# Kernel tuning notes

Measured on AMD Instinct MI355X. Metric: run time of the kernel, lower is better.

The kernel has to match this reference:

```python
import jax, jax.numpy as jnp
import numpy as np

B, S, HD, NH, AH, F = 64, 256, 512, 8, 256, 2
DH = HD // NH          # item/pos head dim = 64
DA = AH // NH          # attribute head dim = 32
EPS = 1e-12


def setup_inputs() -> dict:
    key = jax.random.key(0)
    ks = iter(jax.random.split(key, 32))
    rn = lambda shape, s=1.0: jax.random.normal(next(ks), shape, dtype=jnp.float32) * s
    w = 0.02
    return {
        "input_tensor": rn((B, S, HD)),
        "attribute_table": rn((B, S, 1, AH)),
        "position_embedding": rn((B, S, HD)),
        "Wq": rn((HD, HD), w), "bq": jnp.zeros((HD,), jnp.float32),
        "Wk": rn((HD, HD), w), "bk": jnp.zeros((HD,), jnp.float32),
        "Wv": rn((HD, HD), w), "bv": jnp.zeros((HD,), jnp.float32),
        "Wqp": rn((HD, HD), w), "bqp": jnp.zeros((HD,), jnp.float32),
        "Wkp": rn((HD, HD), w), "bkp": jnp.zeros((HD,), jnp.float32),
        "Wqa": rn((F, AH, AH), w), "bqa": jnp.zeros((F, AH), jnp.float32),
        "Wka": rn((F, AH, AH), w), "bka": jnp.zeros((F, AH), jnp.float32),
        "fw1": rn((S, S), w), "fb1": jnp.zeros((S,), jnp.float32),
        "fw2": rn((1, S), w), "fb2": jnp.zeros((1,), jnp.float32),
        "Wd": rn((HD, HD), w), "bd": jnp.zeros((HD,), jnp.float32),
        "gamma": jnp.ones((HD,), jnp.float32),
        "beta": jnp.zeros((HD,), jnp.float32),
    }


def _split_heads(x, nh):
    b, s, h = x.shape
    return x.reshape(b, s, nh, h // nh).transpose(0, 2, 1, 3)  # [B,H,S,d]


def reference(input_tensor, attribute_table, position_embedding,
              Wq, bq, Wk, bk, Wv, bv, Wqp, bqp, Wkp, bkp,
              Wqa, bqa, Wka, bka, fw1, fb1, fw2, fb2,
              Wd, bd, gamma, beta):
    q = _split_heads(input_tensor @ Wq.T + bq, NH)
    k = _split_heads(input_tensor @ Wk.T + bk, NH)
    v = _split_heads(input_tensor @ Wv.T + bv, NH)
    qp = _split_heads(position_embedding @ Wqp.T + bqp, NH)
    kp = _split_heads(position_embedding @ Wkp.T + bkp, NH)

    item_scores = jnp.einsum('bhqd,bhkd->bhqk', q, k)
    pos_scores = jnp.einsum('bhqd,bhkd->bhqk', qp, kp)

    attr = attribute_table.squeeze(-2)                       # [B,S,AH]
    qa = jnp.einsum('bsc,foc->fbso', attr, Wqa) + bqa[:, None, None, :]
    ka = jnp.einsum('bsc,foc->fbso', attr, Wka) + bka[:, None, None, :]
    qa = qa.reshape(F, B, S, NH, DA).transpose(0, 1, 3, 2, 4)  # [F,B,H,S,da]
    ka = ka.reshape(F, B, S, NH, DA).transpose(0, 1, 3, 2, 4)
    attr_scores = jnp.einsum('fbhqd,fbhkd->fbhqk', qa, ka)
    attr_scores = attr_scores.transpose(1, 2, 3, 0, 4)         # [B,H,S,F,S]

    # gate fusion (VanillaAttention over the F+2 score sources)
    stacked = jnp.concatenate(
        [attr_scores, item_scores[..., None, :], pos_scores[..., None, :]],
        axis=-2)                                               # [B,H,S,F+2,S]
    energy = jnp.maximum(stacked @ fw1.T + fb1, 0.0) @ fw2.T + fb2
    gate_w = jax.nn.softmax(energy.squeeze(-1), axis=-1)        # [B,H,S,F+2]
    scores = jnp.sum(stacked * gate_w[..., None], axis=-2)      # [B,H,S,S]

    scores = scores / np.sqrt(DH).astype(np.float32)
    probs = jax.nn.softmax(scores, axis=-1)
    ctx = jnp.einsum('bhqk,bhkd->bhqd', probs, v)
    ctx = ctx.transpose(0, 2, 1, 3).reshape(B, S, HD)

    h = ctx @ Wd.T + bd
    x = h + input_tensor
    mu = jnp.mean(x, axis=-1, keepdims=True)
    var = jnp.mean(jnp.square(x - mu), axis=-1, keepdims=True)
    return gamma * (x - mu) / jnp.sqrt(var + EPS) + beta
```

## Files before the change

### kernel.cpp

```cpp
#include <hip/hip_runtime.h>

typedef unsigned short u16;
typedef unsigned int   u32;
typedef __bf16 bf16x8 __attribute__((ext_vector_type(8)));
typedef float  f32x4  __attribute__((ext_vector_type(4)));
typedef u16    u16x4  __attribute__((ext_vector_type(4)));
typedef u16    u16x8  __attribute__((ext_vector_type(8)));

#define BB 64
#define SS 256
#define HDIM 512
#define NHEAD 8
#define BS (BB*SS)
#define NBH 512

__device__ __forceinline__ u16 f2bf(float f){
    u32 u = __builtin_bit_cast(u32, f);
    u32 r = u + 0x7FFFu + ((u>>16)&1u);
    return (u16)(r>>16);
}
__device__ __forceinline__ float bf2f(u16 u){
    return __builtin_bit_cast(float, (u32)u<<16);
}
__device__ __forceinline__ void gload16(const void* g, void* l){
    __builtin_amdgcn_global_load_lds(
        (const __attribute__((address_space(1))) void*)g,
        (__attribute__((address_space(3))) void*)l, 16, 0, 0);
}

__device__ __forceinline__ size_t zrow(int bh, int s){
    return ((size_t)bh*256 + s)*384;
}

__global__ __launch_bounds__(256) void cvt_k(const float* __restrict__ s,
                                             u16* __restrict__ d, int n8)
{
    int i = blockIdx.x*256 + threadIdx.x;
    const int stride = gridDim.x*256;
    for (; i < n8; i += stride) {
        f32x4 a = ((const f32x4*)s)[i*2];
        f32x4 b = ((const f32x4*)s)[i*2+1];
        u16x8 o = { f2bf(a[0]),f2bf(a[1]),f2bf(a[2]),f2bf(a[3]),
                    f2bf(b[0]),f2bf(b[1]),f2bf(b[2]),f2bf(b[3]) };
        ((u16x8*)d)[i] = o;
    }
}

__global__ __launch_bounds__(256) void cvtW_k(
    const float* __restrict__ Wq,  const float* __restrict__ Wk,
    const float* __restrict__ Wv,  const float* __restrict__ Wqp,
    const float* __restrict__ Wkp, const float* __restrict__ Wqa,
    const float* __restrict__ Wka, const float* __restrict__ Wd,
    u16* __restrict__ dst)
{
    const int i = blockIdx.x*256 + threadIdx.x;
    const float* s; u16* d; int local;
    if (i < 163840) {
        const int seg = i >> 15; local = i & 32767;
        s = seg==0?Wq:seg==1?Wk:seg==2?Wv:seg==3?Wqp:Wkp;
        d = dst + (size_t)seg*262144;
    } else if (i < 196608) {
        const int j = i - 163840; const int seg = j >> 14; local = j & 16383;
        s = seg ? Wka : Wqa;
        d = dst + 1310720 + (size_t)seg*131072;
    } else {
        local = i - 196608;
        s = Wd; d = dst + 1572864;
    }
    f32x4 a = ((const f32x4*)s)[local*2];
    f32x4 b = ((const f32x4*)s)[local*2+1];
    u16x8 o = { f2bf(a[0]),f2bf(a[1]),f2bf(a[2]),f2bf(a[3]),
                f2bf(b[0]),f2bf(b[1]),f2bf(b[2]),f2bf(b[3]) };
    ((u16x8*)d)[local] = o;
}

__global__ __launch_bounds__(64) void prep_fw1(const float* __restrict__ fw1,
                                               u16* __restrict__ fw1b)
{
    const int row = blockIdx.x;
    const int c0  = threadIdx.x * 4;
    float4 v = *(const float4*)(fw1 + (size_t)row*256 + c0);
    u16x4 pk = { f2bf(v.x), f2bf(v.y), f2bf(v.z), f2bf(v.w) };
    *(u16x4*)((char*)fw1b + (size_t)row*512 + ((c0*2) ^ ((row&7)<<4))) = pk;
}

template<int OUTMODE, int BBF16>
__global__ __launch_bounds__(256,3) void gemm128(
    const u16* __restrict__ A, const void* __restrict__ Bv,
    void* __restrict__ o0, void* __restrict__ o1, void* __restrict__ o2,
    const float* __restrict__ b0, const float* __restrict__ b1,
    const float* __restrict__ b2, const float* __restrict__ resid,
    int N, int K)
{
    __shared__ char sA[16384];
    __shared__ char sB[16384];
    const int tid = threadIdx.x, lane = tid & 63, w = tid >> 6;
    const int wr = (w & 1) * 64, wc = (w >> 1) * 64;
    const int flat = blockIdx.x;
    const int xcd = flat & 7, bi2 = flat >> 3;
    const int n_i = bi2 >> 4, mIn = bi2 & 15;
    const int m0 = (xcd*16 + mIn)*128, n0 = n_i*128;

    f32x4 acc[4][4];
    #pragma unroll
    for (int mi = 0; mi < 4; mi++)
        #pragma unroll
        for (int ni = 0; ni < 4; ni++) acc[mi][ni] = (f32x4){0.f,0.f,0.f,0.f};

    for (int k0 = 0; k0 < K; k0 += 64) {
        __syncthreads();
        #pragma unroll
        for (int i = 0; i < 4; i++) {
            const int off = w*4096 + i*1024 + lane*16;
            const int r = off >> 7, c = off & 0x70;
            gload16(A + (size_t)(m0 + r)*K + k0 + ((c ^ ((r&7)<<4)) >> 1),
                    sA + w*4096 + i*1024);
        }
        if (BBF16) {
            const u16* B = (const u16*)Bv;
            #pragma unroll
            for (int i = 0; i < 4; i++) {
                const int off = w*4096 + i*1024 + lane*16;
                const int r = off >> 7, c = off & 0x70;
                gload16(B + (size_t)(n0 + r)*K + k0 + ((c ^ ((r&7)<<4)) >> 1),
                        sB + w*4096 + i*1024);
            }
        } else {
            const float* B = (const float*)Bv;
            const int r = tid >> 1, cseg = (tid & 1) * 32;
            const float* p = B + (size_t)(n0 + r)*K + k0 + cseg;
            alignas(16) u16 tmp[32];
            #pragma unroll
            for (int j = 0; j < 8; j++) {
                float4 fv = ((const float4*)p)[j];
                tmp[j*4+0]=f2bf(fv.x); tmp[j*4+1]=f2bf(fv.y);
                tmp[j*4+2]=f2bf(fv.z); tmp[j*4+3]=f2bf(fv.w);
            }
            const int rx = (r&7)<<4;
            #pragma unroll
            for (int j = 0; j < 4; j++)
                *(u16x8*)(sB + r*128 + ((cseg*2 + j*16) ^ rx)) = *(u16x8*)(tmp + j*8);
        }
        __syncthreads();
        #pragma unroll
        for (int ks = 0; ks < 2; ks++) {
            const int kb = ks*64 + (lane>>4)*16;
            bf16x8 af[4], bf[4];
            #pragma unroll
            for (int mi = 0; mi < 4; mi++) {
                const int r = wr + mi*16 + (lane&15);
                af[mi] = *(const bf16x8*)(sA + r*128 + (kb ^ ((r&7)<<4)));
            }
            #pragma unroll
            for (int ni = 0; ni < 4; ni++) {
                const int r = wc + ni*16 + (lane&15);
                bf[ni] = *(const bf16x8*)(sB + r*128 + (kb ^ ((r&7)<<4)));
            }
            #pragma unroll
            for (int mi = 0; mi < 4; mi++)
                #pragma unroll
                for (int ni = 0; ni < 4; ni++)
                    acc[mi][ni] = __builtin_amdgcn_mfma_f32_16x16x32_bf16(
                        af[mi], bf[ni], acc[mi][ni], 0,0,0);
        }
    }
    #pragma unroll
    for (int mi = 0; mi < 4; mi++) {
        const int rowb = m0 + wr + mi*16 + (lane>>4)*4;
        const int bi = rowb >> 8, s0 = rowb & 255;
        #pragma unroll
        for (int ni = 0; ni < 4; ni++) {
            const int gn = n0 + wc + ni*16 + (lane&15);
            if (OUTMODE == 2) {
                float* out = (float*)o0;
                const float bb = b0[gn];
                #pragma unroll
                for (int r = 0; r < 4; r++) {
                    size_t idx = (size_t)(rowb+r)*N + gn;
                    out[idx] = acc[mi][ni][r] + bb + resid[idx];
                }
            } else if (OUTMODE == 4) {
                const int seg = gn >> 9, o = gn & 511;
                const int hh = o >> 6, d = o & 63;
                const float bb = (seg==0?b0:seg==1?b1:b2)[o];
                const int bh = bi*8 + hh;
                if (seg < 2) {
                    char* outp = (char*)(seg ? o1 : o0);
                    #pragma unroll
                    for (int r = 0; r < 4; r++) {
                        const int s = s0 + r;
                        *(u16*)(outp + zrow(bh,s) + ((d*2) ^ ((s&7)<<4)))
                            = f2bf(acc[mi][ni][r] + bb);
                    }
                } else {
                    u16x4 pk;
                    #pragma unroll
                    for (int r = 0; r < 4; r++) pk[r] = f2bf(acc[mi][ni][r] + bb);
                    *(u16x4*)((char*)o2 + (size_t)bh*32768 + d*512
                                        + ((s0*2) ^ ((d&7)<<4))) = pk;
                }
            } else if (OUTMODE == 5) {
                const int seg = gn >> 9, o = gn & 511;
                const int hh = o >> 6, d = o & 63;
                const float bb = (seg ? b1 : b0)[o];
                const int bh = bi*8 + hh;
                char* outp = (char*)(seg ? o1 : o0);
                #pragma unroll
                for (int r = 0; r < 4; r++) {
                    const int s = s0 + r;
                    *(u16*)(outp + zrow(bh,s) + (((64+d)*2) ^ ((s&7)<<4)))
                        = f2bf(acc[mi][ni][r] + bb);
                }
            } else {
                const int qk = gn >> 9, fo = gn & 511;
                const int f = fo >> 8, o = fo & 255;
                const int hh = o >> 5, d = o & 31;
                const int cb = 128 + f*32;
                const float bb = (qk ? b1 : b0)[fo];
                const int bh = bi*8 + hh;
                char* outp = (char*)(qk ? o1 : o0);
                #pragma unroll
                for (int r = 0; r < 4; r++) {
                    const int s = s0 + r;
                    *(u16*)(outp + zrow(bh,s) + (((cb+d)*2) ^ ((s&7)<<4)))
                        = f2bf(acc[mi][ni][r] + bb);
                }
            }
        }
    }
}

#define K34B_QZ   53248
#define K34B_QZSZ 13312
#define K34B_SMEM (53248 + 2*13312)

__global__ __launch_bounds__(512,4) void k34b(
    const u16* __restrict__ QZ, const u16* __restrict__ KZ,
    const u16* __restrict__ fw1b, const float* __restrict__ fb1,
    const float* __restrict__ fw2, float* __restrict__ e)
{
    extern __shared__ char sm[];
    const int tid = threadIdx.x, lane = tid & 63, w = tid >> 6;
    const int bh = blockIdx.x >> 1, sp = blockIdx.x & 1;
    const int l15 = lane & 15, lq = lane >> 4;
    const int base0 = sp ? 64 : 0;
    const int base1 = sp ? 160 : 128;

    auto stage_qz = [&](int qt4, int buf) {
        char* dst = sm + K34B_QZ + buf*K34B_QZSZ;
        {
            const int li = w*64 + lane;
            const int q = li / 13, c = li - q*13;
            const int cc = (c == 12) ? 0 : c;
            const int ld = cc*8;
            const int gd = (ld < 64) ? base0 + ld : base1 + (ld - 64);
            gload16((const char*)QZ + zrow(bh, qt4*64 + q)
                        + ((gd*2) ^ ((q&7)<<4)),
                    dst + w*1024);
        }
        if (w < 5) {
            const int li = 512 + w*64 + lane;
            const int q = li / 13, c = li - q*13;
            const int cc = (c == 12) ? 0 : c;
            const int ld = cc*8;
            const int gd = (ld < 64) ? base0 + ld : base1 + (ld - 64);
            gload16((const char*)QZ + zrow(bh, qt4*64 + q)
                        + ((gd*2) ^ ((q&7)<<4)),
                    dst + 8192 + w*1024);
        }
    };

    stage_qz(0, 0);
    {
        const int spair = tid & 127, dg = tid >> 7;
        const int s0 = spair*2;
        const char* r0 = (const char*)KZ + zrow(bh, s0);
        const char* r1 = (const char*)KZ + zrow(bh, s0+1);
        const int sw0 = (s0&7)<<4, sw1 = ((s0+1)&7)<<4;
        #pragma unroll
        for (int m = 0; m < 3; m++) {
            const int ld0 = dg*24 + m*8;
            const int gd = (ld0 < 64) ? base0 + ld0 : base1 + (ld0 - 64);
            u16x8 v0 = *(const u16x8*)(r0 + ((gd*2) ^ sw0));
            u16x8 v1 = *(const u16x8*)(r1 + ((gd*2) ^ sw1));
            #pragma unroll
            for (int ee = 0; ee < 8; ee++) {
                const int d = ld0 + ee;
                *(u32*)(sm + d*512 + ((s0*2) ^ ((d&7)<<4)))
                    = (u32)v0[ee] | ((u32)v1[ee] << 16);
            }
        }
    }
    __syncthreads();

    const int jb = w & 3, dh = w >> 2;
    f32x4 kacc[4][3];
    #pragma unroll
    for (int js = 0; js < 4; js++)
        #pragma unroll
        for (int ni = 0; ni < 3; ni++) kacc[js][ni] = (f32x4){0.f,0.f,0.f,0.f};
    #pragma unroll
    for (int ks = 0; ks < 8; ks++) {
        const int kb = ks*64 + lq*16;
        bf16x8 a[4];
        #pragma unroll
        for (int js = 0; js < 4; js++) {
            const int ar = jb*64 + js*16 + l15;
            a[js] = *(const bf16x8*)((const char*)fw1b + (size_t)ar*512
                                     + (kb ^ ((l15&7)<<4)));
        }
        #pragma unroll
        for (int ni = 0; ni < 3; ni++) {
            const int dr = dh*48 + ni*16 + l15;
            bf16x8 b = *(const bf16x8*)(sm + dr*512 + (kb ^ ((dr&7)<<4)));
            #pragma unroll
            for (int js = 0; js < 4; js++)
                kacc[js][ni] = __builtin_amdgcn_mfma_f32_16x16x32_bf16(
                    a[js], b, kacc[js][ni], 0,0,0);
        }
    }
    __syncthreads();

    #pragma unroll
    for (int js = 0; js < 4; js++)
        #pragma unroll
        for (int ni = 0; ni < 3; ni++) {
            const int d = dh*48 + ni*16 + l15;
            #pragma unroll
            for (int r = 0; r < 4; r++) {
                const int j = jb*64 + js*16 + lq*4 + r;
                *(u16*)(sm + j*208 + d*2) = f2bf(kacc[js][ni][r]);
            }
        }
    __syncthreads();

    const int qh = w >> 2;
    bf16x8 af2[4][3];
    #pragma unroll
    for (int js = 0; js < 4; js++) {
        const int ar = jb*64 + js*16 + l15;
        #pragma unroll
        for (int ks = 0; ks < 3; ks++)
            af2[js][ks] = *(const bf16x8*)(sm + ar*208 + ks*64 + lq*16);
    }
    float f1v[4][4], f2v[4][4];
    #pragma unroll
    for (int js = 0; js < 4; js++)
        #pragma unroll
        for (int r = 0; r < 4; r++) {
            const int j = jb*64 + js*16 + lq*4 + r;
            f1v[js][r] = fb1[j]; f2v[js][r] = fw2[j];
        }

    for (int qt = 0; qt < 4; qt++) {
        __syncthreads();
        if (qt < 3) stage_qz(qt+1, (qt+1)&1);
        const char* qb = sm + K34B_QZ + (qt&1)*K34B_QZSZ;
        #pragma unroll
        for (int qs = 0; qs < 2; qs++) {
            const int qoff = (qh*32 + qs*16 + l15)*208 + lq*16;
            f32x4 acc[4];
            #pragma unroll
            for (int js = 0; js < 4; js++) acc[js] = (f32x4){0.f,0.f,0.f,0.f};
            #pragma unroll
            for (int kk = 0; kk < 2; kk++) {
                bf16x8 b = *(const bf16x8*)(qb + qoff + kk*64);
                #pragma unroll
                for (int js = 0; js < 4; js++)
                    acc[js] = __builtin_amdgcn_mfma_f32_16x16x32_bf16(
                        af2[js][kk], b, acc[js], 0,0,0);
            }
            {
                float ep = 0.f;
                #pragma unroll
                for (int js = 0; js < 4; js++)
                    #pragma unroll
                    for (int r = 0; r < 4; r++)
                        ep += fmaxf(acc[js][r] + f1v[js][r], 0.f) * f2v[js][r];
                ep += __shfl_xor(ep, 16);
                ep += __shfl_xor(ep, 32);
                if (lane < 16)
                    ((float*)sm)[(jb*2 + 0)*256 + qt*64 + qh*32 + qs*16 + lane] = ep;
            }
            #pragma unroll
            for (int js = 0; js < 4; js++) acc[js] = (f32x4){0.f,0.f,0.f,0.f};
            {
                bf16x8 b = *(const bf16x8*)(qb + qoff + 128);
                #pragma unroll
                for (int js = 0; js < 4; js++)
                    acc[js] = __builtin_amdgcn_mfma_f32_16x16x32_bf16(
                        af2[js][2], b, acc[js], 0,0,0);
            }
            {
                float ep = 0.f;
                #pragma unroll
                for (int js = 0; js < 4; js++)
                    #pragma unroll
                    for (int r = 0; r < 4; r++)
                        ep += fmaxf(acc[js][r] + f1v[js][r], 0.f) * f2v[js][r];
                ep += __shfl_xor(ep, 16);
                ep += __shfl_xor(ep, 32);
                if (lane < 16)
                    ((float*)sm)[(jb*2 + 1)*256 + qt*64 + qh*32 + qs*16 + lane] = ep;
            }
        }
    }
    __syncthreads();
    {
        const int q = tid & 255, sl = tid >> 8;
        const float* el = (const float*)sm;
        float s = 0.f;
        #pragma unroll
        for (int j2 = 0; j2 < 4; j2++) s += el[(j2*2 + sl)*256 + q];
        const int gsrc = sl ? (2 + sp) : sp;
        e[((size_t)bh*256 + q)*4 + gsrc] = s;
    }
}

#define K5_KZ 24576
#define K5_VT 49152
#define K5_SMEM 81920

__global__ __launch_bounds__(256,2) void k5_mix(
    const u16* __restrict__ QZ, const u16* __restrict__ KZ,
    const u16* __restrict__ VT, const float* __restrict__ e,
    u16* __restrict__ ctx)
{
    extern __shared__ char sm[];
    const int tid = threadIdx.x, lane = tid & 63, w = tid >> 6;
    const int flat = blockIdx.x;
    const int xcd = flat & 7, idx = flat >> 3;
    const int qt = idx & 3;
    const int bh = (idx >> 2) * 8 + xcd;
    const int q0 = qt*64;
    const int b = bh >> 3, h = bh & 7;
    const int kq16 = (lane>>4)*16;

    #pragma unroll
    for (int i = 0; i < 6; i++)
        gload16((const char*)QZ + zrow(bh, q0) + i*4096 + w*1024 + lane*16,
                sm + i*4096 + w*1024);
    #pragma unroll
    for (int i = 0; i < 8; i++)
        gload16((const char*)VT + (size_t)bh*32768 + i*4096 + w*1024 + lane*16,
                sm + K5_VT + i*4096 + w*1024);
    #pragma unroll
    for (int i = 0; i < 6; i++)
        gload16((const char*)KZ + zrow(bh, 0) + i*4096 + w*1024 + lane*16,
                sm + K5_KZ + i*4096 + w*1024);
    __syncthreads();

    const int qrow = w*16 + (lane&15);
    float ga[4];
    {
        f32x4 ev = *(const f32x4*)(e + ((size_t)bh*256 + q0 + qrow)*4);
        float em = fmaxf(fmaxf(ev[0],ev[1]), fmaxf(ev[2],ev[3]));
        float s = 0.f;
        #pragma unroll
        for (int j = 0; j < 4; j++) { ga[j] = __expf(ev[j]-em); s += ga[j]; }
        const float gi = 1.f / s;
        #pragma unroll
        for (int j = 0; j < 4; j++) ga[j] *= gi;
    }
    const int asw = ((lane&15)&7) << 4;
    bf16x8 aF[6];
    #pragma unroll
    for (int ks = 0; ks < 6; ks++) {
        const int sidx = (ks<2)?0:(ks<4)?1:(ks<5)?2:3;
        u16x8 v = *(const u16x8*)(sm + qrow*384 + ((ks*64 + kq16) ^ asw));
        const float gg = ga[sidx];
        u16x8 pk;
        #pragma unroll
        for (int j = 0; j < 8; j++) pk[j] = f2bf(bf2f(v[j]) * gg);
        aF[ks] = __builtin_bit_cast(bf16x8, pk);
    }

    f32x4 macc[4][4];
    #pragma unroll
    for (int kt = 0; kt < 4; kt++)
        #pragma unroll
        for (int n = 0; n < 4; n++) macc[kt][n] = (f32x4){0.f,0.f,0.f,0.f};
    u16x8 kreg[6];
    #pragma unroll
    for (int kt = 0; kt < 4; kt++) {
        if (kt < 3) {
            #pragma unroll
            for (int j = 0; j < 6; j++)
                kreg[j] = *(const u16x8*)((const char*)KZ + zrow(bh, (kt+1)*64)
                                          + (tid + j*256)*16);
        }
        #pragma unroll
        for (int n = 0; n < 4; n++) {
            const int kr = n*16 + (lane&15);
            const int ksw = (kr&7)<<4;
            #pragma unroll
            for (int ks = 0; ks < 6; ks++) {
                bf16x8 bb = *(const bf16x8*)(sm + K5_KZ + kr*384 + ((ks*64 + kq16) ^ ksw));
                macc[kt][n] = __builtin_amdgcn_mfma_f32_16x16x32_bf16(
                    aF[ks], bb, macc[kt][n], 0,0,0);
            }
        }
        if (kt < 3) {
            __syncthreads();
            #pragma unroll
            for (int j = 0; j < 6; j++)
                *(u16x8*)(sm + K5_KZ + (tid + j*256)*16) = kreg[j];
            __syncthreads();
        }
    }
    __syncthreads();

    #pragma unroll
    for (int rr = 0; rr < 4; rr++) {
        float mx = -3.4e38f;
        #pragma unroll
        for (int kt = 0; kt < 4; kt++)
            #pragma unroll
            for (int n = 0; n < 4; n++) mx = fmaxf(mx, macc[kt][n][rr]);
        #pragma unroll
        for (int msk = 1; msk < 16; msk <<= 1) mx = fmaxf(mx, __shfl_xor(mx, msk));
        float s = 0.f;
        #pragma unroll
        for (int kt = 0; kt < 4; kt++)
            #pragma unroll
            for (int n = 0; n < 4; n++) {
                float pv = __expf((macc[kt][n][rr] - mx) * 0.125f);
                macc[kt][n][rr] = pv; s += pv;
            }
        #pragma unroll
        for (int msk = 1; msk < 16; msk <<= 1) s += __shfl_xor(s, msk);
        const float inv = 1.f / s;
        const int orow = w*16 + (lane>>4)*4 + rr;
        const int osw = (orow&7)<<4;
        #pragma unroll
        for (int kt = 0; kt < 4; kt++)
            #pragma unroll
            for (int n = 0; n < 4; n++) {
                const int col = kt*64 + n*16 + (lane&15);
                *(u16*)(sm + orow*512 + ((col*2) ^ osw)) = f2bf(macc[kt][n][rr]*inv);
            }
    }
    __syncthreads();

    f32x4 pacc[4];
    #pragma unroll
    for (int n = 0; n < 4; n++) pacc[n] = (f32x4){0.f,0.f,0.f,0.f};
    const int prow = w*16 + (lane&15);
    const int psw = ((lane&15)&7)<<4;
    #pragma unroll
    for (int ks = 0; ks < 8; ks++) {
        const int kb = ks*64 + kq16;
        bf16x8 a = *(const bf16x8*)(sm + prow*512 + (kb ^ psw));
        #pragma unroll
        for (int n = 0; n < 4; n++) {
            const int dr = n*16 + (lane&15);
            bf16x8 bb = *(const bf16x8*)(sm + K5_VT + dr*512 + (kb ^ ((dr&7)<<4)));
            pacc[n] = __builtin_amdgcn_mfma_f32_16x16x32_bf16(a, bb, pacc[n], 0,0,0);
        }
    }
    {
        const int orow = w*16 + (lane>>4)*4;
        #pragma unroll
        for (int n = 0; n < 4; n++) {
            const int d = n*16 + (lane&15);
            #pragma unroll
            for (int r = 0; r < 4; r++) {
                const size_t grow = (size_t)b*256 + q0 + orow + r;
                ctx[grow*512 + h*64 + d] = f2bf(pacc[n][r]);
            }
        }
    }
}

__global__ __launch_bounds__(256) void ln_k(float* __restrict__ x,
    const float* __restrict__ gamma, const float* __restrict__ beta)
{
    const int row = blockIdx.x*4 + (threadIdx.x >> 6);
    const int l = threadIdx.x & 63;
    float* p = x + (size_t)row*HDIM;
    f32x4 v0 = *(const f32x4*)(p + l*4);
    f32x4 v1 = *(const f32x4*)(p + 256 + l*4);
    float s = v0[0]+v0[1]+v0[2]+v0[3] + v1[0]+v1[1]+v1[2]+v1[3];
    #pragma unroll
    for (int msk = 1; msk < 64; msk <<= 1) s += __shfl_xor(s, msk);
    const float mu = s * (1.f/512.f);
    float vs = 0.f;
    #pragma unroll
    for (int j = 0; j < 4; j++) {
        float d0 = v0[j]-mu, d1 = v1[j]-mu;
        vs += d0*d0 + d1*d1;
    }
    #pragma unroll
    for (int msk = 1; msk < 64; msk <<= 1) vs += __shfl_xor(vs, msk);
    const float inv = 1.f / sqrtf(vs * (1.f/512.f) + 1e-12f);
    f32x4 o0, o1;
    #pragma unroll
    for (int j = 0; j < 4; j++) {
        o0[j] = gamma[l*4+j]     * (v0[j]-mu) * inv + beta[l*4+j];
        o1[j] = gamma[256+l*4+j] * (v1[j]-mu) * inv + beta[256+l*4+j];
    }
    *(f32x4*)(p + l*4) = o0;
    *(f32x4*)(p + 256 + l*4) = o1;
}

extern "C" void kernel_launch(void* const* d_in, const int* in_sizes, int n_in,
                              void* d_out, int out_size, void* d_ws, size_t ws_size,
                              hipStream_t stream)
{
    const float* input = (const float*)d_in[0];
    const float* attrt = (const float*)d_in[1];
    const float* pose  = (const float*)d_in[2];
    const float* Wq  = (const float*)d_in[3];  const float* bq  = (const float*)d_in[4];
    const float* Wk  = (const float*)d_in[5];  const float* bk  = (const float*)d_in[6];
    const float* Wv  = (const float*)d_in[7];  const float* bv  = (const float*)d_in[8];
    const float* Wqp = (const float*)d_in[9];  const float* bqp = (const float*)d_in[10];
    const float* Wkp = (const float*)d_in[11]; const float* bkp = (const float*)d_in[12];
    const float* Wqa = (const float*)d_in[13]; const float* bqa = (const float*)d_in[14];
    const float* Wka = (const float*)d_in[15]; const float* bka = (const float*)d_in[16];
    const float* fw1 = (const float*)d_in[17]; const float* fb1 = (const float*)d_in[18];
    const float* fw2 = (const float*)d_in[19];
    const float* Wd  = (const float*)d_in[21]; const float* bd  = (const float*)d_in[22];
    const float* gamma = (const float*)d_in[23]; const float* beta = (const float*)d_in[24];

    char* ws = (char*)d_ws;
    u16*   wsQZ  = (u16*)(ws);
    u16*   wsKZ  = (u16*)(ws + 50331648);
    u16*   wsTmp = (u16*)(ws + 100663296);
    float* wsE   = (float*)(ws + 117440512);
    u16*   fw1b  = (u16*)(ws + 119537664);
    u16*   dW    = (u16*)(ws + 119668736);
    u16*   wsVT  = (u16*)d_out;

    dim3 blk(256);

    cvtW_k<<<dim3(896), blk, 0, stream>>>(Wq, Wk, Wv, Wqp, Wkp, Wqa, Wka, Wd, dW);
    prep_fw1<<<dim3(256), dim3(64), 0, stream>>>(fw1, fw1b);

    cvt_k<<<dim3(2048), blk, 0, stream>>>(attrt, wsTmp, 524288);
    gemm128<6,1><<<dim3(1024), blk, 0, stream>>>(wsTmp, dW + 1310720,
        wsQZ, wsKZ, nullptr, bqa, bka, nullptr, nullptr, 1024, 256);
    cvt_k<<<dim3(2048), blk, 0, stream>>>(input, wsTmp, 1048576);
    gemm128<4,1><<<dim3(1536), blk, 0, stream>>>(wsTmp, dW,
        wsQZ, wsKZ, wsVT, bq, bk, bv, nullptr, 1536, 512);
    cvt_k<<<dim3(2048), blk, 0, stream>>>(pose, wsTmp, 1048576);
    gemm128<5,1><<<dim3(1024), blk, 0, stream>>>(wsTmp, dW + 786432,
        wsQZ, wsKZ, nullptr, bqp, bkp, nullptr, nullptr, 1024, 512);

    hipFuncSetAttribute(reinterpret_cast<const void*>(k34b),
                        hipFuncAttributeMaxDynamicSharedMemorySize, K34B_SMEM);
    k34b<<<dim3(NBH*2), dim3(512), K34B_SMEM, stream>>>(wsQZ, wsKZ, fw1b, fb1, fw2, wsE);

    hipFuncSetAttribute(reinterpret_cast<const void*>(k5_mix),
                        hipFuncAttributeMaxDynamicSharedMemorySize, K5_SMEM);
    k5_mix<<<dim3(2048), blk, K5_SMEM, stream>>>(wsQZ, wsKZ, wsVT, wsE, wsTmp);

    gemm128<2,1><<<dim3(512), blk, 0, stream>>>(wsTmp, dW + 1572864,
        d_out, nullptr, nullptr, bd, nullptr, nullptr, input, 512, 512);
    ln_k<<<dim3(BS/4), blk, 0, stream>>>((float*)d_out, gamma, beta);
}
```

Baseline: 237.3 us.

## Fuse fp32 activation conversion into projection GEMMs by swapping operand roles

Removes the three standalone fp32→bf16 conversion kernels for attribute, input and position tensors. The projection GEMMs now take the bf16 weights as the A operand and read the fp32 activations directly as B through the existing non-bf16 B path, computing the transposed product. The epilogues are rewritten so each lane holds four consecutive output features, which allows vectorized bias loads and packed u16x4 stores for Q/K tiles. The aim is to save the conversion traffic and kernel launches, at the cost of converting fp32 inside the GEMM loop and scattered scalar stores for the transposed V output.

```diff
diff --git a/kernel.cpp b/kernel.cpp
--- a/kernel.cpp
+++ b/kernel.cpp
@@ -30,20 +30,6 @@
 
 __device__ __forceinline__ size_t zrow(int bh, int s){
     return ((size_t)bh*256 + s)*384;
-}
-
-__global__ __launch_bounds__(256) void cvt_k(const float* __restrict__ s,
-                                             u16* __restrict__ d, int n8)
-{
-    int i = blockIdx.x*256 + threadIdx.x;
-    const int stride = gridDim.x*256;
-    for (; i < n8; i += stride) {
-        f32x4 a = ((const f32x4*)s)[i*2];
-        f32x4 b = ((const f32x4*)s)[i*2+1];
-        u16x8 o = { f2bf(a[0]),f2bf(a[1]),f2bf(a[2]),f2bf(a[3]),
-                    f2bf(b[0]),f2bf(b[1]),f2bf(b[2]),f2bf(b[3]) };
-        ((u16x8*)d)[i] = o;
-    }
 }
 
 __global__ __launch_bounds__(256) void cvtW_k(
@@ -98,8 +84,12 @@
     const int wr = (w & 1) * 64, wc = (w >> 1) * 64;
     const int flat = blockIdx.x;
     const int xcd = flat & 7, bi2 = flat >> 3;
-    const int n_i = bi2 >> 4, mIn = bi2 & 15;
-    const int m0 = (xcd*16 + mIn)*128, n0 = n_i*128;
+    int m0, n0;
+    if (OUTMODE == 2) {
+        m0 = (xcd*16 + (bi2 & 15))*128; n0 = (bi2 >> 4)*128;
+    } else {
+        n0 = (xcd*16 + (bi2 & 15))*128; m0 = (bi2 >> 4)*128;
+    }
 
     f32x4 acc[4][4];
     #pragma unroll
@@ -164,14 +154,14 @@
                         af[mi], bf[ni], acc[mi][ni], 0,0,0);
         }
     }
-    #pragma unroll
-    for (int mi = 0; mi < 4; mi++) {
-        const int rowb = m0 + wr + mi*16 + (lane>>4)*4;
-        const int bi = rowb >> 8, s0 = rowb & 255;
-        #pragma unroll
-        for (int ni = 0; ni < 4; ni++) {
-            const int gn = n0 + wc + ni*16 + (lane&15);
-            if (OUTMODE == 2) {
+
+    if (OUTMODE == 2) {
+        #pragma unroll
+        for (int mi = 0; mi < 4; mi++) {
+            const int rowb = m0 + wr + mi*16 + (lane>>4)*4;
+            #pragma unroll
+            for (int ni = 0; ni < 4; ni++) {
+                const int gn = n0 + wc + ni*16 + (lane&15);
                 float* out = (float*)o0;
                 const float bb = b0[gn];
                 #pragma unroll
@@ -179,51 +169,69 @@
                     size_t idx = (size_t)(rowb+r)*N + gn;
                     out[idx] = acc[mi][ni][r] + bb + resid[idx];
                 }
-            } else if (OUTMODE == 4) {
-                const int seg = gn >> 9, o = gn & 511;
-                const int hh = o >> 6, d = o & 63;
-                const float bb = (seg==0?b0:seg==1?b1:b2)[o];
-                const int bh = bi*8 + hh;
-                if (seg < 2) {
-                    char* outp = (char*)(seg ? o1 : o0);
-                    #pragma unroll
-                    for (int r = 0; r < 4; r++) {
-                        const int s = s0 + r;
-                        *(u16*)(outp + zrow(bh,s) + ((d*2) ^ ((s&7)<<4)))
-                            = f2bf(acc[mi][ni][r] + bb);
+            }
+        }
+    } else {
+        #pragma unroll
+        for (int mi = 0; mi < 4; mi++) {
+            const int fb = m0 + wr + mi*16 + (lane>>4)*4;
+            if (OUTMODE == 4) {
+                const int seg = fb >> 9, o = fb & 511;
+                const int hh = o >> 6, d0 = o & 63;
+                const float* bp = seg==0?b0:seg==1?b1:b2;
+                const f32x4 bb4 = *(const f32x4*)(bp + o);
+                #pragma unroll
+                for (int ni = 0; ni < 4; ni++) {
+                    const int sn = n0 + wc + ni*16 + (lane&15);
+                    const int bi = sn >> 8, s = sn & 255;
+                    const int bh = bi*8 + hh;
+                    if (seg < 2) {
+                        char* outp = (char*)(seg ? o1 : o0);
+                        u16x4 pk;
+                        #pragma unroll
+                        for (int r = 0; r < 4; r++) pk[r] = f2bf(acc[mi][ni][r] + bb4[r]);
+                        *(u16x4*)(outp + zrow(bh,s) + ((d0*2) ^ ((s&7)<<4))) = pk;
+                    } else {
+                        #pragma unroll
+                        for (int r = 0; r < 4; r++) {
+                            const int d = d0 + r;
+                            *(u16*)((char*)o2 + (size_t)bh*32768 + d*512
+                                              + ((s*2) ^ ((d&7)<<4)))
+                                = f2bf(acc[mi][ni][r] + bb4[r]);
+                        }
                     }
-                } else {
+                }
+            } else if (OUTMODE == 5) {
+                const int seg = fb >> 9, o = fb & 511;
+                const int hh = o >> 6, d0 = o & 63;
+                const f32x4 bb4 = *(const f32x4*)((seg ? b1 : b0) + o);
+                char* outp = (char*)(seg ? o1 : o0);
+                #pragma unroll
+                for (int ni = 0; ni < 4; ni++) {
+                    const int sn = n0 + wc + ni*16 + (lane&15);
+                    const int bi = sn >> 8, s = sn & 255;
+                    const int bh = bi*8 + hh;
                     u16x4 pk;
                     #pragma unroll
-                    for (int r = 0; r < 4; r++) pk[r] = f2bf(acc[mi][ni][r] + bb);
-                    *(u16x4*)((char*)o2 + (size_t)bh*32768 + d*512
-                                        + ((s0*2) ^ ((d&7)<<4))) = pk;
-                }
-            } else if (OUTMODE == 5) {
-                const int seg = gn >> 9, o = gn & 511;
-                const int hh = o >> 6, d = o & 63;
-                const float bb = (seg ? b1 : b0)[o];
-                const int bh = bi*8 + hh;
-                char* outp = (char*)(seg ? o1 : o0);
-                #pragma unroll
-                for (int r = 0; r < 4; r++) {
-                    const int s = s0 + r;
-                    *(u16*)(outp + zrow(bh,s) + (((64+d)*2) ^ ((s&7)<<4)))
-                        = f2bf(acc[mi][ni][r] + bb);
+                    for (int r = 0; r < 4; r++) pk[r] = f2bf(acc[mi][ni][r] + bb4[r]);
+                    *(u16x4*)(outp + zrow(bh,s) + (((64+d0)*2) ^ ((s&7)<<4))) = pk;
                 }
             } else {
-                const int qk = gn >> 9, fo = gn & 511;
-                const int f = fo >> 8, o = fo & 255;
-                const int hh = o >> 5, d = o & 31;
-                const int cb = 128 + f*32;
-                const float bb = (qk ? b1 : b0)[fo];
-                const int bh = bi*8 + hh;
+                const int qk = fb >> 9, fo = fb & 511;
+                const int ff = fo >> 8, o = fo & 255;
+                const int hh = o >> 5, d0 = o & 31;
+                const int cb = 128 + ff*32;
+                const f32x4 bb4 = *(const f32x4*)((qk ? b1 : b0) + fo);
                 char* outp = (char*)(qk ? o1 : o0);
                 #pragma unroll
-                for (int r = 0; r < 4; r++) {
-                    const int s = s0 + r;
-                    *(u16*)(outp + zrow(bh,s) + (((cb+d)*2) ^ ((s&7)<<4)))
-                        = f2bf(acc[mi][ni][r] + bb);
+                for (int ni = 0; ni < 4; ni++) {
+                    const int sn = n0 + wc + ni*16 + (lane&15);
+                    const int bi = sn >> 8, s = sn & 255;
+                    const int bh = bi*8 + hh;
+                    u16x4 pk;
+                    #pragma unroll
+                    for (int r = 0; r < 4; r++) pk[r] = f2bf(acc[mi][ni][r] + bb4[r]);
+                    *(u16x4*)(outp + zrow(bh,s) + (((cb+d0)*2) ^ ((s&7)<<4))) = pk;
                 }
             }
         }
@@ -636,14 +644,11 @@
     cvtW_k<<<dim3(896), blk, 0, stream>>>(Wq, Wk, Wv, Wqp, Wkp, Wqa, Wka, Wd, dW);
     prep_fw1<<<dim3(256), dim3(64), 0, stream>>>(fw1, fw1b);
 
-    cvt_k<<<dim3(2048), blk, 0, stream>>>(attrt, wsTmp, 524288);
-    gemm128<6,1><<<dim3(1024), blk, 0, stream>>>(wsTmp, dW + 1310720,
+    gemm128<6,0><<<dim3(1024), blk, 0, stream>>>(dW + 1310720, attrt,
         wsQZ, wsKZ, nullptr, bqa, bka, nullptr, nullptr, 1024, 256);
-    cvt_k<<<dim3(2048), blk, 0, stream>>>(input, wsTmp, 1048576);
-    gemm128<4,1><<<dim3(1536), blk, 0, stream>>>(wsTmp, dW,
+    gemm128<4,0><<<dim3(1536), blk, 0, stream>>>(dW, input,
         wsQZ, wsKZ, wsVT, bq, bk, bv, nullptr, 1536, 512);
-    cvt_k<<<dim3(2048), blk, 0, stream>>>(pose, wsTmp, 1048576);
-    gemm128<5,1><<<dim3(1024), blk, 0, stream>>>(wsTmp, dW + 786432,
+    gemm128<5,0><<<dim3(1024), blk, 0, stream>>>(dW + 786432, pose,
         wsQZ, wsKZ, nullptr, bqp, bkp, nullptr, nullptr, 1024, 512);
 
     hipFuncSetAttribute(reinterpret_cast<const void*>(k34b),
```

Result: slower. 278.1 us (+17.2%).

## Shrink k5 LDS footprint with smaller K chunks and streamed V tiles for occupancy

Applied to the files above, without the earlier changes.

The mixing kernel now stages K in 32-row chunks (8 iterations instead of 4) and streams V^T in double-buffered 16-row tiles during the PV step instead of loading all of V^T up front. This cuts dynamic shared memory from 80KB to 52KB so launch bounds can request 3 blocks per CU instead of 2. In exchange it adds more __syncthreads barriers and smaller, less overlapped load phases, and register pressure may rise from keeping 8 A fragments live.

```diff
diff --git a/kernel.cpp b/kernel.cpp
--- a/kernel.cpp
+++ b/kernel.cpp
@@ -418,10 +418,10 @@
 }
 
 #define K5_KZ 24576
-#define K5_VT 49152
-#define K5_SMEM 81920
-
-__global__ __launch_bounds__(256,2) void k5_mix(
+#define K5_VT 36864
+#define K5_SMEM 53248
+
+__global__ __launch_bounds__(256,3) void k5b(
     const u16* __restrict__ QZ, const u16* __restrict__ KZ,
     const u16* __restrict__ VT, const float* __restrict__ e,
     u16* __restrict__ ctx)
@@ -435,19 +435,19 @@
     const int q0 = qt*64;
     const int b = bh >> 3, h = bh & 7;
     const int kq16 = (lane>>4)*16;
+    const char* QZc = (const char*)QZ + zrow(bh, q0);
+    const char* KZc = (const char*)KZ + zrow(bh, 0);
+    const char* VTc = (const char*)VT + (size_t)bh*32768;
 
     #pragma unroll
     for (int i = 0; i < 6; i++)
-        gload16((const char*)QZ + zrow(bh, q0) + i*4096 + w*1024 + lane*16,
-                sm + i*4096 + w*1024);
-    #pragma unroll
-    for (int i = 0; i < 8; i++)
-        gload16((const char*)VT + (size_t)bh*32768 + i*4096 + w*1024 + lane*16,
-                sm + K5_VT + i*4096 + w*1024);
-    #pragma unroll
-    for (int i = 0; i < 6; i++)
-        gload16((const char*)KZ + zrow(bh, 0) + i*4096 + w*1024 + lane*16,
-                sm + K5_KZ + i*4096 + w*1024);
+        gload16(QZc + i*4096 + tid*16, sm + i*4096 + tid*16);
+    #pragma unroll
+    for (int i = 0; i < 3; i++)
+        gload16(KZc + i*4096 + tid*16, sm + K5_KZ + i*4096 + tid*16);
+    #pragma unroll
+    for (int i = 0; i < 2; i++)
+        gload16(VTc + i*4096 + tid*16, sm + K5_VT + i*4096 + tid*16);
     __syncthreads();
 
     const int qrow = w*16 + (lane&15);
@@ -475,35 +475,34 @@
         aF[ks] = __builtin_bit_cast(bf16x8, pk);
     }
 
-    f32x4 macc[4][4];
-    #pragma unroll
-    for (int kt = 0; kt < 4; kt++)
-        #pragma unroll
-        for (int n = 0; n < 4; n++) macc[kt][n] = (f32x4){0.f,0.f,0.f,0.f};
-    u16x8 kreg[6];
-    #pragma unroll
-    for (int kt = 0; kt < 4; kt++) {
-        if (kt < 3) {
-            #pragma unroll
-            for (int j = 0; j < 6; j++)
-                kreg[j] = *(const u16x8*)((const char*)KZ + zrow(bh, (kt+1)*64)
+    f32x4 macc[16];
+    #pragma unroll
+    for (int t = 0; t < 16; t++) macc[t] = (f32x4){0.f,0.f,0.f,0.f};
+    u16x8 kreg[3];
+    #pragma unroll
+    for (int kt = 0; kt < 8; kt++) {
+        if (kt < 7) {
+            #pragma unroll
+            for (int j = 0; j < 3; j++)
+                kreg[j] = *(const u16x8*)(KZc + (size_t)(kt+1)*12288
                                           + (tid + j*256)*16);
         }
         #pragma unroll
-        for (int n = 0; n < 4; n++) {
-            const int kr = n*16 + (lane&15);
+        for (int n2 = 0; n2 < 2; n2++) {
+            const int kr = n2*16 + (lane&15);
             const int ksw = (kr&7)<<4;
             #pragma unroll
             for (int ks = 0; ks < 6; ks++) {
-                bf16x8 bb = *(const bf16x8*)(sm + K5_KZ + kr*384 + ((ks*64 + kq16) ^ ksw));
-                macc[kt][n] = __builtin_amdgcn_mfma_f32_16x16x32_bf16(
-                    aF[ks], bb, macc[kt][n], 0,0,0);
-            }
-        }
-        if (kt < 3) {
+                bf16x8 bb = *(const bf16x8*)(sm + K5_KZ + kr*384
+                                             + ((ks*64 + kq16) ^ ksw));
+                macc[kt*2+n2] = __builtin_amdgcn_mfma_f32_16x16x32_bf16(
+                    aF[ks], bb, macc[kt*2+n2], 0,0,0);
+            }
+        }
+        if (kt < 7) {
             __syncthreads();
             #pragma unroll
-            for (int j = 0; j < 6; j++)
+            for (int j = 0; j < 3; j++)
                 *(u16x8*)(sm + K5_KZ + (tid + j*256)*16) = kreg[j];
             __syncthreads();
         }
@@ -514,61 +513,62 @@
     for (int rr = 0; rr < 4; rr++) {
         float mx = -3.4e38f;
         #pragma unroll
-        for (int kt = 0; kt < 4; kt++)
-            #pragma unroll
-            for (int n = 0; n < 4; n++) mx = fmaxf(mx, macc[kt][n][rr]);
+        for (int t = 0; t < 16; t++) mx = fmaxf(mx, macc[t][rr]);
         #pragma unroll
         for (int msk = 1; msk < 16; msk <<= 1) mx = fmaxf(mx, __shfl_xor(mx, msk));
         float s = 0.f;
         #pragma unroll
-        for (int kt = 0; kt < 4; kt++)
-            #pragma unroll
-            for (int n = 0; n < 4; n++) {
-                float pv = __expf((macc[kt][n][rr] - mx) * 0.125f);
-                macc[kt][n][rr] = pv; s += pv;
-            }
+        for (int t = 0; t < 16; t++) {
+            float pv = __expf((macc[t][rr] - mx) * 0.125f);
+            macc[t][rr] = pv; s += pv;
+        }
         #pragma unroll
         for (int msk = 1; msk < 16; msk <<= 1) s += __shfl_xor(s, msk);
         const float inv = 1.f / s;
         const int orow = w*16 + (lane>>4)*4 + rr;
         const int osw = (orow&7)<<4;
         #pragma unroll
-        for (int kt = 0; kt < 4; kt++)
-            #pragma unroll
-            for (int n = 0; n < 4; n++) {
-                const int col = kt*64 + n*16 + (lane&15);
-                *(u16*)(sm + orow*512 + ((col*2) ^ osw)) = f2bf(macc[kt][n][rr]*inv);
-            }
+        for (int t = 0; t < 16; t++) {
+            const int col = t*16 + (lane&15);
+            *(u16*)(sm + orow*512 + ((col*2) ^ osw)) = f2bf(macc[t][rr]*inv);
+        }
     }
     __syncthreads();
 
-    f32x4 pacc[4];
-    #pragma unroll
-    for (int n = 0; n < 4; n++) pacc[n] = (f32x4){0.f,0.f,0.f,0.f};
+    bf16x8 a[8];
     const int prow = w*16 + (lane&15);
     const int psw = ((lane&15)&7)<<4;
     #pragma unroll
-    for (int ks = 0; ks < 8; ks++) {
-        const int kb = ks*64 + kq16;
-        bf16x8 a = *(const bf16x8*)(sm + prow*512 + (kb ^ psw));
-        #pragma unroll
-        for (int n = 0; n < 4; n++) {
-            const int dr = n*16 + (lane&15);
-            bf16x8 bb = *(const bf16x8*)(sm + K5_VT + dr*512 + (kb ^ ((dr&7)<<4)));
-            pacc[n] = __builtin_amdgcn_mfma_f32_16x16x32_bf16(a, bb, pacc[n], 0,0,0);
-        }
-    }
-    {
-        const int orow = w*16 + (lane>>4)*4;
-        #pragma unroll
-        for (int n = 0; n < 4; n++) {
-            const int d = n*16 + (lane&15);
+    for (int ks = 0; ks < 8; ks++)
+        a[ks] = *(const bf16x8*)(sm + prow*512 + ((ks*64 + kq16) ^ psw));
+
+    const int orow = w*16 + (lane>>4)*4;
+    #pragma unroll
+    for (int n = 0; n < 4; n++) {
+        if (n < 3) {
+            #pragma unroll
+            for (int i = 0; i < 2; i++)
+                gload16(VTc + (size_t)(n+1)*8192 + i*4096 + tid*16,
+                        sm + K5_VT + ((n+1)&1)*8192 + i*4096 + tid*16);
+        }
+        f32x4 pacc = (f32x4){0.f,0.f,0.f,0.f};
+        const char* vb = sm + K5_VT + (n&1)*8192;
+        const int dl = lane & 15;
+        const int vsw = (dl&7)<<4;
+        #pragma unroll
+        for (int ks = 0; ks < 8; ks++) {
+            bf16x8 bb = *(const bf16x8*)(vb + dl*512 + ((ks*64 + kq16) ^ vsw));
+            pacc = __builtin_amdgcn_mfma_f32_16x16x32_bf16(a[ks], bb, pacc, 0,0,0);
+        }
+        {
+            const int d = n*16 + dl;
             #pragma unroll
             for (int r = 0; r < 4; r++) {
                 const size_t grow = (size_t)b*256 + q0 + orow + r;
-                ctx[grow*512 + h*64 + d] = f2bf(pacc[n][r]);
-            }
-        }
+                ctx[grow*512 + h*64 + d] = f2bf(pacc[r]);
+            }
+        }
+        if (n < 3) __syncthreads();
     }
 }
 
@@ -650,9 +650,9 @@
                         hipFuncAttributeMaxDynamicSharedMemorySize, K34B_SMEM);
     k34b<<<dim3(NBH*2), dim3(512), K34B_SMEM, stream>>>(wsQZ, wsKZ, fw1b, fb1, fw2, wsE);
 
-    hipFuncSetAttribute(reinterpret_cast<const void*>(k5_mix),
+    hipFuncSetAttribute(reinterpret_cast<const void*>(k5b),
                         hipFuncAttributeMaxDynamicSharedMemorySize, K5_SMEM);
-    k5_mix<<<dim3(2048), blk, K5_SMEM, stream>>>(wsQZ, wsKZ, wsVT, wsE, wsTmp);
+    k5b<<<dim3(2048), blk, K5_SMEM, stream>>>(wsQZ, wsKZ, wsVT, wsE, wsTmp);
 
     gemm128<2,1><<<dim3(512), blk, 0, stream>>>(wsTmp, dW + 1572864,
         d_out, nullptr, nullptr, bd, nullptr, nullptr, input, 512, 512);
```

After: 234.5 us. No clear change (-1.2%).
